# Kernel optimization log

Measured on AMD Instinct MI355X. Metric: run time of the kernel, lower is better.

## Reference

```python
import jax, jax.numpy as jnp
import numpy as np
from jax import lax

WINDOW_SIZE = 11
SIGMA = 1.5
C1 = 0.01 ** 2
C2 = 0.03 ** 2


def _gaussian_window(window_size: int, sigma: float) -> jnp.ndarray:
    coords = jnp.arange(window_size, dtype=jnp.float32) - window_size // 2
    g = jnp.exp(-0.5 * (coords / sigma) ** 2)
    g = g / g.sum()
    return g[:, None] * g[None, :]  # (ws, ws)


def _dwconv(x, win2d):
    # x: (B, C, H, W); win2d: (ws, ws). Depthwise conv, same padding.
    c = x.shape[1]
    ws = win2d.shape[0]
    pad = ws // 2
    k = jnp.broadcast_to(win2d[None, None], (c, 1, ws, ws))  # (O=C, I/g=1, ws, ws)
    return lax.conv_general_dilated(
        x, k, window_strides=(1, 1), padding=[(pad, pad), (pad, pad)],
        dimension_numbers=('NCHW', 'OIHW', 'NCHW'), feature_group_count=c)


def setup_inputs() -> dict:
    key = jax.random.key(0)
    k1, k2 = jax.random.split(key)
    shape = (32, 3, 512, 512)
    img1 = jax.random.uniform(k1, shape, dtype=jnp.float32)
    img2 = jax.random.uniform(k2, shape, dtype=jnp.float32)
    return {"img1": img1, "img2": img2}


def reference(img1, img2):
    win = _gaussian_window(WINDOW_SIZE, SIGMA).astype(img1.dtype)
    mu1 = _dwconv(img1, win)
    mu2 = _dwconv(img2, win)
    mu1_sq = mu1 * mu1
    mu2_sq = mu2 * mu2
    mu12 = mu1 * mu2
    sigma1_sq = _dwconv(img1 * img1, win) - mu1_sq
    sigma2_sq = _dwconv(img2 * img2, win) - mu2_sq
    sigma12 = _dwconv(img1 * img2, win) - mu12
    numerator = (2.0 * mu12 + C1) * (2.0 * sigma12 + C2)
    denominator = (mu1_sq + mu2_sq + C1) * (sigma1_sq + sigma2_sq + C2)
    ssim_map = numerator / denominator
    return 1.0 - ssim_map.mean()
```

## Files before the change

### kernel.cpp

```cpp
#include <hip/hip_runtime.h>

#define IMG   512
#define TW    32
#define TH    32
#define HALO  5
#define WS    11
#define IHH   42
#define LDW   36
#define SIGSZ (IHH*LDW)
#define NP    96
#define NSLOT 256

__global__ __launch_bounds__(256, 5) void ssim_main(const float* __restrict__ img1,
                                                    const float* __restrict__ img2,
                                                    double* __restrict__ acc) {
    constexpr float W[WS] = {
        0.00102837990674f, 0.00759883148699f, 0.03600079242909f,
        0.10936069869137f, 0.21300538108707f, 0.26601190869814f,
        0.21300538108707f, 0.10936069869137f, 0.03600079242909f,
        0.00759883148699f, 0.00102837990674f };

    __shared__ float hA[5 * SIGSZ];

    const int tid = threadIdx.x;
    const int bx = blockIdx.x;
    const int by = blockIdx.y;
    const float* p1 = img1 + (size_t)blockIdx.z * (IMG*IMG);
    const float* p2 = img2 + (size_t)blockIdx.z * (IMG*IMG);

    if (tid < IHH * 4) {
        const int r  = tid >> 2;
        const int ch = tid & 3;
        const int gy = by * TH + r - HALO;
        const bool rowOK = (unsigned)gy < IMG;
        const float* r1 = p1 + (size_t)gy * IMG;
        const float* r2 = p2 + (size_t)gy * IMG;

        float a1[8], a2[8], a11[8], a22[8], a12[8];
        #pragma unroll
        for (int o = 0; o < 8; ++o) { a1[o]=0.f; a2[o]=0.f; a11[o]=0.f; a22[o]=0.f; a12[o]=0.f; }

        #pragma unroll
        for (int j = 0; j < 6; ++j) {
            const int gx = bx * TW + ch * 8 - 8 + 4 * j;
            float4 A = make_float4(0.f,0.f,0.f,0.f), B = A;
            if (rowOK && (unsigned)gx < IMG) {
                A = *(const float4*)(r1 + gx);
                B = *(const float4*)(r2 + gx);
            }
            const float e1[4] = {A.x,A.y,A.z,A.w};
            const float e2[4] = {B.x,B.y,B.z,B.w};
            #pragma unroll
            for (int e = 0; e < 4; ++e) {
                const int i = 4*j + e;
                if (i < 3 || i > 20) continue;
                const float x1 = e1[e], x2 = e2[e];
                const float q11 = x1*x1, q22 = x2*x2, q12 = x1*x2;
                #pragma unroll
                for (int o = 0; o < 8; ++o) {
                    const int t = i - 3 - o;
                    if (t >= 0 && t < WS) {
                        a1[o]  += W[t]*x1;  a2[o]  += W[t]*x2;
                        a11[o] += W[t]*q11; a22[o] += W[t]*q22; a12[o] += W[t]*q12;
                    }
                }
            }
        }

        const int wb = r * LDW + ch * 8;
        *(float4*)&hA[0*SIGSZ + wb]     = make_float4(a1[0],a1[1],a1[2],a1[3]);
        *(float4*)&hA[0*SIGSZ + wb + 4] = make_float4(a1[4],a1[5],a1[6],a1[7]);
        *(float4*)&hA[1*SIGSZ + wb]     = make_float4(a2[0],a2[1],a2[2],a2[3]);
        *(float4*)&hA[1*SIGSZ + wb + 4] = make_float4(a2[4],a2[5],a2[6],a2[7]);
        *(float4*)&hA[2*SIGSZ + wb]     = make_float4(a11[0],a11[1],a11[2],a11[3]);
        *(float4*)&hA[2*SIGSZ + wb + 4] = make_float4(a11[4],a11[5],a11[6],a11[7]);
        *(float4*)&hA[3*SIGSZ + wb]     = make_float4(a22[0],a22[1],a22[2],a22[3]);
        *(float4*)&hA[3*SIGSZ + wb + 4] = make_float4(a22[4],a22[5],a22[6],a22[7]);
        *(float4*)&hA[4*SIGSZ + wb]     = make_float4(a12[0],a12[1],a12[2],a12[3]);
        *(float4*)&hA[4*SIGSZ + wb + 4] = make_float4(a12[4],a12[5],a12[6],a12[7]);
    }
    __syncthreads();

    const int c  = tid & 31;
    const int r0 = (tid >> 5) << 2;
    float m[5][4];
    #pragma unroll
    for (int s = 0; s < 5; ++s)
        #pragma unroll
        for (int o = 0; o < 4; ++o) m[s][o] = 0.f;

    #pragma unroll
    for (int s = 0; s < 5; ++s) {
        int off = s * SIGSZ + r0 * LDW + c;
        asm("" : "+v"(off));
        #pragma unroll
        for (int k = 0; k < 8; ++k) {
            const float h = hA[off + k * LDW];
            #pragma unroll
            for (int o = 0; o < 4; ++o) {
                const int t = k - o;
                if (t >= 0 && t < WS) m[s][o] += W[t] * h;
            }
        }
        int off2 = off + 8 * LDW;
        asm("" : "+v"(off2));
        #pragma unroll
        for (int k = 8; k < 14; ++k) {
            const float h = hA[off2 + (k - 8) * LDW];
            #pragma unroll
            for (int o = 0; o < 4; ++o) {
                const int t = k - o;
                if (t >= 0 && t < WS) m[s][o] += W[t] * h;
            }
        }
    }

    const float C1 = 0.01f*0.01f, C2 = 0.03f*0.03f;
    float lsum = 0.f;
    #pragma unroll
    for (int o = 0; o < 4; ++o) {
        const float mu1 = m[0][o], mu2 = m[1][o];
        const float mu1s = mu1*mu1, mu2s = mu2*mu2, mu12 = mu1*mu2;
        const float s11 = m[2][o] - mu1s;
        const float s22 = m[3][o] - mu2s;
        const float s12 = m[4][o] - mu12;
        const float num = (2.f*mu12 + C1) * (2.f*s12 + C2);
        const float den = (mu1s + mu2s + C1) * (s11 + s22 + C2);
        lsum += num * __builtin_amdgcn_rcpf(den);
    }

    #pragma unroll
    for (int d = 32; d >= 1; d >>= 1)
        lsum += __shfl_down(lsum, d, 64);
    __shared__ float wsum[4];
    if ((tid & 63) == 0) wsum[tid >> 6] = lsum;
    __syncthreads();
    if (tid == 0) {
        const float t = wsum[0] + wsum[1] + wsum[2] + wsum[3];
        const int slot = (blockIdx.z * 256 + blockIdx.y * 16 + blockIdx.x) & (NSLOT - 1);
        atomicAdd(&acc[slot], (double)t);
    }
}

__global__ void ssim_final(const double* __restrict__ acc, float* __restrict__ out) {
    const int l = threadIdx.x;
    double s = acc[l] + acc[l + 64] + acc[l + 128] + acc[l + 192];
    #pragma unroll
    for (int d = 32; d >= 1; d >>= 1)
        s += __shfl_down(s, d, 64);
    if (l == 0)
        out[0] = 1.0f - (float)(s / (double)((size_t)NP * IMG * IMG));
}

extern "C" void kernel_launch(void* const* d_in, const int* in_sizes, int n_in,
                              void* d_out, int out_size, void* d_ws, size_t ws_size,
                              hipStream_t stream) {
    const float* img1 = (const float*)d_in[0];
    const float* img2 = (const float*)d_in[1];
    float* out = (float*)d_out;
    double* acc = (double*)d_ws;

    hipMemsetAsync(d_ws, 0, NSLOT * sizeof(double), stream);

    dim3 grid(IMG / TW, IMG / TH, NP);
    ssim_main<<<grid, dim3(256), 0, stream>>>(img1, img2, acc);
    ssim_final<<<1, dim3(64), 0, stream>>>(acc, out);
}
```

Measured before the change: 116.4 us.

## Compute vertical Gaussian pass with bf16 MFMA using hi/lo split weights

The vertical blur pass is recast as a banded matrix product. A small kernel builds a Toeplitz Gaussian matrix split into bf16 hi and lo parts, and the horizontal partial sums are stored to LDS as bf16 and fed to 32x32x16 MFMA instructions. Blocks shrink to a single 64-lane wave, so each wave now does the horizontal pass for all 42 rows. Rounding the intermediate sums to bf16 lowers precision and may hurt the variance terms. The smaller blocks also change occupancy and how much work each wave does serially.

```diff
diff --git a/kernel.cpp b/kernel.cpp
--- a/kernel.cpp
+++ b/kernel.cpp
@@ -1,37 +1,71 @@
 #include <hip/hip_runtime.h>
+#include <hip/hip_bf16.h>
 
 #define IMG   512
 #define TW    32
 #define TH    32
-#define HALO  5
 #define WS    11
-#define IHH   42
-#define LDW   36
-#define SIGSZ (IHH*LDW)
 #define NP    96
 #define NSLOT 256
+#define HROWS 48
+#define HCOLS 36
 
-__global__ __launch_bounds__(256, 5) void ssim_main(const float* __restrict__ img1,
-                                                    const float* __restrict__ img2,
-                                                    double* __restrict__ acc) {
-    constexpr float W[WS] = {
-        0.00102837990674f, 0.00759883148699f, 0.03600079242909f,
-        0.10936069869137f, 0.21300538108707f, 0.26601190869814f,
-        0.21300538108707f, 0.10936069869137f, 0.03600079242909f,
-        0.00759883148699f, 0.00102837990674f };
+typedef __attribute__((ext_vector_type(8)))  short bfrag8;
+typedef __attribute__((ext_vector_type(16))) float facc16;
 
-    __shared__ float hA[5 * SIGSZ];
+#define GAUSS_W { \
+    0.00102837990674f, 0.00759883148699f, 0.03600079242909f, \
+    0.10936069869137f, 0.21300538108707f, 0.26601190869814f, \
+    0.21300538108707f, 0.10936069869137f, 0.03600079242909f, \
+    0.00759883148699f, 0.00102837990674f }
 
-    const int tid = threadIdx.x;
-    const int bx = blockIdx.x;
-    const int by = blockIdx.y;
-    const float* p1 = img1 + (size_t)blockIdx.z * (IMG*IMG);
-    const float* p2 = img2 + (size_t)blockIdx.z * (IMG*IMG);
+static __device__ __forceinline__ ushort f2bf(float x) {
+    __hip_bfloat16 h = __float2bfloat16(x);
+    return __builtin_bit_cast(ushort, h);
+}
 
-    if (tid < IHH * 4) {
-        const int r  = tid >> 2;
-        const int ch = tid & 3;
-        const int gy = by * TH + r - HALO;
+__global__ void build_g(ushort* __restrict__ gw) {
+    constexpr float W[WS] = GAUSS_W;
+    const int lane = threadIdx.x;
+    const int row  = lane & 31;
+    const int kg   = (lane >> 5) * 8;
+    for (int s = 0; s < 3; ++s) {
+        for (int e = 0; e < 8; ++e) {
+            const int k = 16 * s + kg + e;
+            const int d = k - row;
+            float wv = 0.f;
+            #pragma unroll
+            for (int q = 0; q < WS; ++q) if (d == q) wv = W[q];
+            const float hi = __bfloat162float(__float2bfloat16(wv));
+            const float lo = wv - hi;
+            gw[(s * 64 + lane) * 8 + e]        = f2bf(hi);
+            gw[1536 + (s * 64 + lane) * 8 + e] = f2bf(lo);
+        }
+    }
+}
+
+__global__ __launch_bounds__(64) void ssim_main(const float* __restrict__ img1,
+                                                const float* __restrict__ img2,
+                                                const ushort* __restrict__ gw,
+                                                double* __restrict__ acc) {
+    constexpr float W[WS] = GAUSS_W;
+    __shared__ ushort H[5][HROWS][HCOLS];
+
+    const int lane = threadIdx.x;
+    const int bx = blockIdx.x, by = blockIdx.y;
+    const float* p1 = img1 + (size_t)blockIdx.z * (IMG * IMG);
+    const float* p2 = img2 + (size_t)blockIdx.z * (IMG * IMG);
+
+    #pragma unroll
+    for (int s = 0; s < 5; ++s) {
+        uint* zp = (uint*)&H[s][42][0];
+        for (int i = lane; i < 108; i += 64) zp[i] = 0;
+    }
+
+    for (int u = lane; u < 168; u += 64) {
+        const int r  = u >> 2;
+        const int ch = u & 3;
+        const int gy = by * TH + r - 5;
         const bool rowOK = (unsigned)gy < IMG;
         const float* r1 = p1 + (size_t)gy * IMG;
         const float* r2 = p2 + (size_t)gy * IMG;
@@ -67,63 +101,52 @@
             }
         }
 
-        const int wb = r * LDW + ch * 8;
-        *(float4*)&hA[0*SIGSZ + wb]     = make_float4(a1[0],a1[1],a1[2],a1[3]);
-        *(float4*)&hA[0*SIGSZ + wb + 4] = make_float4(a1[4],a1[5],a1[6],a1[7]);
-        *(float4*)&hA[1*SIGSZ + wb]     = make_float4(a2[0],a2[1],a2[2],a2[3]);
-        *(float4*)&hA[1*SIGSZ + wb + 4] = make_float4(a2[4],a2[5],a2[6],a2[7]);
-        *(float4*)&hA[2*SIGSZ + wb]     = make_float4(a11[0],a11[1],a11[2],a11[3]);
-        *(float4*)&hA[2*SIGSZ + wb + 4] = make_float4(a11[4],a11[5],a11[6],a11[7]);
-        *(float4*)&hA[3*SIGSZ + wb]     = make_float4(a22[0],a22[1],a22[2],a22[3]);
-        *(float4*)&hA[3*SIGSZ + wb + 4] = make_float4(a22[4],a22[5],a22[6],a22[7]);
-        *(float4*)&hA[4*SIGSZ + wb]     = make_float4(a12[0],a12[1],a12[2],a12[3]);
-        *(float4*)&hA[4*SIGSZ + wb + 4] = make_float4(a12[4],a12[5],a12[6],a12[7]);
+        #define WRSIG(S, ARR) \
+            *(ushort4*)&H[S][r][ch*8]   = make_ushort4(f2bf(ARR[0]),f2bf(ARR[1]),f2bf(ARR[2]),f2bf(ARR[3])); \
+            *(ushort4*)&H[S][r][ch*8+4] = make_ushort4(f2bf(ARR[4]),f2bf(ARR[5]),f2bf(ARR[6]),f2bf(ARR[7]));
+        WRSIG(0, a1) WRSIG(1, a2) WRSIG(2, a11) WRSIG(3, a22) WRSIG(4, a12)
+        #undef WRSIG
     }
+
+    const bfrag8* gfrag = (const bfrag8*)gw;
+    const bfrag8 ghi0 = gfrag[lane], ghi1 = gfrag[64 + lane], ghi2 = gfrag[128 + lane];
+    const bfrag8 glo0 = gfrag[192 + lane], glo1 = gfrag[256 + lane], glo2 = gfrag[320 + lane];
+
     __syncthreads();
 
-    const int c  = tid & 31;
-    const int r0 = (tid >> 5) << 2;
-    float m[5][4];
-    #pragma unroll
-    for (int s = 0; s < 5; ++s)
-        #pragma unroll
-        for (int o = 0; o < 4; ++o) m[s][o] = 0.f;
+    const int col = lane & 31;
+    const int kg  = (lane >> 5) * 8;
 
+    facc16 accs[5];
     #pragma unroll
     for (int s = 0; s < 5; ++s) {
-        int off = s * SIGSZ + r0 * LDW + c;
-        asm("" : "+v"(off));
-        #pragma unroll
-        for (int k = 0; k < 8; ++k) {
-            const float h = hA[off + k * LDW];
-            #pragma unroll
-            for (int o = 0; o < 4; ++o) {
-                const int t = k - o;
-                if (t >= 0 && t < WS) m[s][o] += W[t] * h;
-            }
-        }
-        int off2 = off + 8 * LDW;
-        asm("" : "+v"(off2));
-        #pragma unroll
-        for (int k = 8; k < 14; ++k) {
-            const float h = hA[off2 + (k - 8) * LDW];
-            #pragma unroll
-            for (int o = 0; o < 4; ++o) {
-                const int t = k - o;
-                if (t >= 0 && t < WS) m[s][o] += W[t] * h;
-            }
-        }
+        facc16 a = {};
+        #define KSTEP(T, GHI, GLO) { \
+            const int kb = 16*T + kg; \
+            union { uint u[4]; bfrag8 v; } bb; \
+            bb.u[0] = (uint)H[s][kb+0][col] | ((uint)H[s][kb+1][col] << 16); \
+            bb.u[1] = (uint)H[s][kb+2][col] | ((uint)H[s][kb+3][col] << 16); \
+            bb.u[2] = (uint)H[s][kb+4][col] | ((uint)H[s][kb+5][col] << 16); \
+            bb.u[3] = (uint)H[s][kb+6][col] | ((uint)H[s][kb+7][col] << 16); \
+            a = __builtin_amdgcn_mfma_f32_32x32x16_bf16(GHI, bb.v, a, 0, 0, 0); \
+            a = __builtin_amdgcn_mfma_f32_32x32x16_bf16(GLO, bb.v, a, 0, 0, 0); }
+        KSTEP(0, ghi0, glo0)
+        KSTEP(1, ghi1, glo1)
+        KSTEP(2, ghi2, glo2)
+        #undef KSTEP
+        accs[s] = a;
     }
 
     const float C1 = 0.01f*0.01f, C2 = 0.03f*0.03f;
     float lsum = 0.f;
     #pragma unroll
-    for (int o = 0; o < 4; ++o) {
-        const float mu1 = m[0][o], mu2 = m[1][o];
+    for (int r = 0; r < 16; ++r) {
+        const float mu1 = accs[0][r], mu2 = accs[1][r];
+        const float m11 = accs[2][r], m22 = accs[3][r], m12 = accs[4][r];
         const float mu1s = mu1*mu1, mu2s = mu2*mu2, mu12 = mu1*mu2;
-        const float s11 = m[2][o] - mu1s;
-        const float s22 = m[3][o] - mu2s;
-        const float s12 = m[4][o] - mu12;
+        const float s11 = m11 - mu1s;
+        const float s22 = m22 - mu2s;
+        const float s12 = m12 - mu12;
         const float num = (2.f*mu12 + C1) * (2.f*s12 + C2);
         const float den = (mu1s + mu2s + C1) * (s11 + s22 + C2);
         lsum += num * __builtin_amdgcn_rcpf(den);
@@ -132,13 +155,9 @@
     #pragma unroll
     for (int d = 32; d >= 1; d >>= 1)
         lsum += __shfl_down(lsum, d, 64);
-    __shared__ float wsum[4];
-    if ((tid & 63) == 0) wsum[tid >> 6] = lsum;
-    __syncthreads();
-    if (tid == 0) {
-        const float t = wsum[0] + wsum[1] + wsum[2] + wsum[3];
+    if (lane == 0) {
         const int slot = (blockIdx.z * 256 + blockIdx.y * 16 + blockIdx.x) & (NSLOT - 1);
-        atomicAdd(&acc[slot], (double)t);
+        atomicAdd(&acc[slot], (double)lsum);
     }
 }
 
@@ -159,10 +178,12 @@
     const float* img2 = (const float*)d_in[1];
     float* out = (float*)d_out;
     double* acc = (double*)d_ws;
+    ushort* gw = (ushort*)((char*)d_ws + NSLOT * sizeof(double));
 
     hipMemsetAsync(d_ws, 0, NSLOT * sizeof(double), stream);
+    build_g<<<1, 64, 0, stream>>>(gw);
 
     dim3 grid(IMG / TW, IMG / TH, NP);
-    ssim_main<<<grid, dim3(256), 0, stream>>>(img1, img2, acc);
+    ssim_main<<<grid, dim3(64), 0, stream>>>(img1, img2, gw, acc);
     ssim_final<<<1, dim3(64), 0, stream>>>(acc, out);
 }
```

Measured after the change: 167.7 us. 1.44x slower.

## Store horizontal partial sums as packed bf16 row pairs on a 64-wide tile

Applied to the files above, without the earlier changes.

The tile widens to 64 columns, and each thread now computes horizontal blur sums for two adjacent rows at 4 output columns each. The results are packed as bf16 pairs into shared memory, which halves LDS footprint and read traffic. The vertical pass reads uint4 vectors and unpacks even and odd rows to produce two output rows per thread. This cuts shared-memory bandwidth and gives more work per block, at the cost of bf16 rounding of intermediate sums (an accuracy risk, since variance is computed as a difference) and lower occupancy from launch_bounds 4.

```diff
diff --git a/kernel.cpp b/kernel.cpp
--- a/kernel.cpp
+++ b/kernel.cpp
@@ -1,17 +1,30 @@
 #include <hip/hip_runtime.h>
+#include <hip/hip_bf16.h>
 
 #define IMG   512
-#define TW    32
+#define TW    64
 #define TH    32
-#define HALO  5
 #define WS    11
-#define IHH   42
-#define LDW   36
-#define SIGSZ (IHH*LDW)
 #define NP    96
 #define NSLOT 256
+#define PR    21
+#define PLANE (PR*64)
 
-__global__ __launch_bounds__(256, 5) void ssim_main(const float* __restrict__ img1,
+static __device__ __forceinline__ ushort f2bf(float x) {
+    __hip_bfloat16 h = __float2bfloat16(x);
+    return __builtin_bit_cast(ushort, h);
+}
+static __device__ __forceinline__ uint pkbf(float ev, float od) {
+    return (uint)f2bf(ev) | ((uint)f2bf(od) << 16);
+}
+static __device__ __forceinline__ float bflo(uint v) {
+    return __builtin_bit_cast(float, v << 16);
+}
+static __device__ __forceinline__ float bfhi(uint v) {
+    return __builtin_bit_cast(float, v & 0xffff0000u);
+}
+
+__global__ __launch_bounds__(256, 4) void ssim_main(const float* __restrict__ img1,
                                                     const float* __restrict__ img2,
                                                     double* __restrict__ acc) {
     constexpr float W[WS] = {
@@ -20,97 +33,97 @@
         0.21300538108707f, 0.10936069869137f, 0.03600079242909f,
         0.00759883148699f, 0.00102837990674f };
 
-    __shared__ float hA[5 * SIGSZ];
+    __shared__ uint HP[5 * PLANE];
 
     const int tid = threadIdx.x;
     const int bx = blockIdx.x;
     const int by = blockIdx.y;
-    const float* p1 = img1 + (size_t)blockIdx.z * (IMG*IMG);
-    const float* p2 = img2 + (size_t)blockIdx.z * (IMG*IMG);
+    const float* p1 = img1 + (size_t)blockIdx.z * (IMG * IMG);
+    const float* p2 = img2 + (size_t)blockIdx.z * (IMG * IMG);
 
-    if (tid < IHH * 4) {
-        const int r  = tid >> 2;
-        const int ch = tid & 3;
-        const int gy = by * TH + r - HALO;
-        const bool rowOK = (unsigned)gy < IMG;
-        const float* r1 = p1 + (size_t)gy * IMG;
-        const float* r2 = p2 + (size_t)gy * IMG;
+    for (int u = tid; u < PR * 16; u += 256) {
+        const int pr = u >> 4;
+        const int cg = u & 15;
 
-        float a1[8], a2[8], a11[8], a22[8], a12[8];
+        float A[5][2][4];
         #pragma unroll
-        for (int o = 0; o < 8; ++o) { a1[o]=0.f; a2[o]=0.f; a11[o]=0.f; a22[o]=0.f; a12[o]=0.f; }
+        for (int s = 0; s < 5; ++s)
+            #pragma unroll
+            for (int rw = 0; rw < 2; ++rw)
+                #pragma unroll
+                for (int o = 0; o < 4; ++o) A[s][rw][o] = 0.f;
 
         #pragma unroll
-        for (int j = 0; j < 6; ++j) {
-            const int gx = bx * TW + ch * 8 - 8 + 4 * j;
-            float4 A = make_float4(0.f,0.f,0.f,0.f), B = A;
-            if (rowOK && (unsigned)gx < IMG) {
-                A = *(const float4*)(r1 + gx);
-                B = *(const float4*)(r2 + gx);
-            }
-            const float e1[4] = {A.x,A.y,A.z,A.w};
-            const float e2[4] = {B.x,B.y,B.z,B.w};
+        for (int rw = 0; rw < 2; ++rw) {
+            const int gy = by * TH + 2 * pr + rw - 5;
+            const bool rowOK = (unsigned)gy < IMG;
+            const float* r1 = p1 + (size_t)gy * IMG;
+            const float* r2 = p2 + (size_t)gy * IMG;
             #pragma unroll
-            for (int e = 0; e < 4; ++e) {
-                const int i = 4*j + e;
-                if (i < 3 || i > 20) continue;
-                const float x1 = e1[e], x2 = e2[e];
-                const float q11 = x1*x1, q22 = x2*x2, q12 = x1*x2;
+            for (int j = 0; j < 5; ++j) {
+                const int gx = bx * TW + cg * 4 - 8 + 4 * j;
+                float4 X = make_float4(0.f,0.f,0.f,0.f), Y = X;
+                if (rowOK && (unsigned)gx < IMG) {
+                    X = *(const float4*)(r1 + gx);
+                    Y = *(const float4*)(r2 + gx);
+                }
+                const float e1[4] = {X.x,X.y,X.z,X.w};
+                const float e2[4] = {Y.x,Y.y,Y.z,Y.w};
                 #pragma unroll
-                for (int o = 0; o < 8; ++o) {
-                    const int t = i - 3 - o;
-                    if (t >= 0 && t < WS) {
-                        a1[o]  += W[t]*x1;  a2[o]  += W[t]*x2;
-                        a11[o] += W[t]*q11; a22[o] += W[t]*q22; a12[o] += W[t]*q12;
+                for (int e = 0; e < 4; ++e) {
+                    const int i = 4*j + e;
+                    if (i < 3 || i > 16) continue;
+                    const float x1 = e1[e], x2 = e2[e];
+                    const float q11 = x1*x1, q22 = x2*x2, q12 = x1*x2;
+                    #pragma unroll
+                    for (int o = 0; o < 4; ++o) {
+                        const int t = i - 3 - o;
+                        if (t >= 0 && t < WS) {
+                            A[0][rw][o] += W[t]*x1;  A[1][rw][o] += W[t]*x2;
+                            A[2][rw][o] += W[t]*q11; A[3][rw][o] += W[t]*q22;
+                            A[4][rw][o] += W[t]*q12;
+                        }
                     }
                 }
             }
         }
 
-        const int wb = r * LDW + ch * 8;
-        *(float4*)&hA[0*SIGSZ + wb]     = make_float4(a1[0],a1[1],a1[2],a1[3]);
-        *(float4*)&hA[0*SIGSZ + wb + 4] = make_float4(a1[4],a1[5],a1[6],a1[7]);
-        *(float4*)&hA[1*SIGSZ + wb]     = make_float4(a2[0],a2[1],a2[2],a2[3]);
-        *(float4*)&hA[1*SIGSZ + wb + 4] = make_float4(a2[4],a2[5],a2[6],a2[7]);
-        *(float4*)&hA[2*SIGSZ + wb]     = make_float4(a11[0],a11[1],a11[2],a11[3]);
-        *(float4*)&hA[2*SIGSZ + wb + 4] = make_float4(a11[4],a11[5],a11[6],a11[7]);
-        *(float4*)&hA[3*SIGSZ + wb]     = make_float4(a22[0],a22[1],a22[2],a22[3]);
-        *(float4*)&hA[3*SIGSZ + wb + 4] = make_float4(a22[4],a22[5],a22[6],a22[7]);
-        *(float4*)&hA[4*SIGSZ + wb]     = make_float4(a12[0],a12[1],a12[2],a12[3]);
-        *(float4*)&hA[4*SIGSZ + wb + 4] = make_float4(a12[4],a12[5],a12[6],a12[7]);
+        #pragma unroll
+        for (int s = 0; s < 5; ++s) {
+            const uint4 pv = make_uint4(pkbf(A[s][0][0], A[s][1][0]),
+                                        pkbf(A[s][0][1], A[s][1][1]),
+                                        pkbf(A[s][0][2], A[s][1][2]),
+                                        pkbf(A[s][0][3], A[s][1][3]));
+            *(uint4*)&HP[(s * PR + pr) * 64 + cg * 4] = pv;
+        }
     }
     __syncthreads();
 
-    const int c  = tid & 31;
-    const int r0 = (tid >> 5) << 2;
-    float m[5][4];
+    const int q0 = tid >> 4;
+    const int cg = tid & 15;
+
+    float m[5][2][4];
     #pragma unroll
     for (int s = 0; s < 5; ++s)
         #pragma unroll
-        for (int o = 0; o < 4; ++o) m[s][o] = 0.f;
+        for (int pth = 0; pth < 2; ++pth)
+            #pragma unroll
+            for (int c = 0; c < 4; ++c) m[s][pth][c] = 0.f;
 
     #pragma unroll
     for (int s = 0; s < 5; ++s) {
-        int off = s * SIGSZ + r0 * LDW + c;
-        asm("" : "+v"(off));
         #pragma unroll
-        for (int k = 0; k < 8; ++k) {
-            const float h = hA[off + k * LDW];
+        for (int j = 0; j <= 5; ++j) {
+            const uint4 v = *(const uint4*)&HP[(s * PR + q0 + j) * 64 + cg * 4];
+            const uint vv[4] = {v.x, v.y, v.z, v.w};
             #pragma unroll
-            for (int o = 0; o < 4; ++o) {
-                const int t = k - o;
-                if (t >= 0 && t < WS) m[s][o] += W[t] * h;
-            }
-        }
-        int off2 = off + 8 * LDW;
-        asm("" : "+v"(off2));
-        #pragma unroll
-        for (int k = 8; k < 14; ++k) {
-            const float h = hA[off2 + (k - 8) * LDW];
-            #pragma unroll
-            for (int o = 0; o < 4; ++o) {
-                const int t = k - o;
-                if (t >= 0 && t < WS) m[s][o] += W[t] * h;
+            for (int c = 0; c < 4; ++c) {
+                const float lo = bflo(vv[c]);
+                const float hi = bfhi(vv[c]);
+                if (2*j < WS)     m[s][0][c] += W[2*j] * lo;
+                if (2*j+1 < WS)   m[s][0][c] += W[2*j+1] * hi;
+                if (2*j-1 >= 0)   m[s][1][c] += W[2*j-1] * lo;
+                if (2*j < WS)     m[s][1][c] += W[2*j] * hi;
             }
         }
     }
@@ -118,15 +131,18 @@
     const float C1 = 0.01f*0.01f, C2 = 0.03f*0.03f;
     float lsum = 0.f;
     #pragma unroll
-    for (int o = 0; o < 4; ++o) {
-        const float mu1 = m[0][o], mu2 = m[1][o];
-        const float mu1s = mu1*mu1, mu2s = mu2*mu2, mu12 = mu1*mu2;
-        const float s11 = m[2][o] - mu1s;
-        const float s22 = m[3][o] - mu2s;
-        const float s12 = m[4][o] - mu12;
-        const float num = (2.f*mu12 + C1) * (2.f*s12 + C2);
-        const float den = (mu1s + mu2s + C1) * (s11 + s22 + C2);
-        lsum += num * __builtin_amdgcn_rcpf(den);
+    for (int pth = 0; pth < 2; ++pth) {
+        #pragma unroll
+        for (int c = 0; c < 4; ++c) {
+            const float mu1 = m[0][pth][c], mu2 = m[1][pth][c];
+            const float mu1s = mu1*mu1, mu2s = mu2*mu2, mu12 = mu1*mu2;
+            const float s11 = m[2][pth][c] - mu1s;
+            const float s22 = m[3][pth][c] - mu2s;
+            const float s12 = m[4][pth][c] - mu12;
+            const float num = (2.f*mu12 + C1) * (2.f*s12 + C2);
+            const float den = (mu1s + mu2s + C1) * (s11 + s22 + C2);
+            lsum += num * __builtin_amdgcn_rcpf(den);
+        }
     }
 
     #pragma unroll
@@ -137,8 +153,8 @@
     __syncthreads();
     if (tid == 0) {
         const float t = wsum[0] + wsum[1] + wsum[2] + wsum[3];
-        const int slot = (blockIdx.z * 256 + blockIdx.y * 16 + blockIdx.x) & (NSLOT - 1);
-        atomicAdd(&acc[slot], (double)t);
+        const int bid = (blockIdx.z * gridDim.y + blockIdx.y) * gridDim.x + blockIdx.x;
+        atomicAdd(&acc[bid & (NSLOT - 1)], (double)t);
     }
 }
 
```

After: 125.8 us. 8.1% more time.
